# Optimization experiments

Measured on AMD Instinct MI355X. Metric: run time of the kernel, lower is better.

Reference implementation:

```python
import jax, jax.numpy as jnp
import numpy as np

B, T, D, H = 512, 128, 128, 256


def _uniform(key, shape, fan):
    s = 1.0 / np.sqrt(fan)
    return jax.random.uniform(key, shape, minval=-s, maxval=s, dtype=jnp.float32)


def setup_inputs() -> dict:
    key = jax.random.key(0)
    ks = jax.random.split(key, 16)
    return {
        "x": jax.random.normal(ks[0], (B, T, D), jnp.float32),
        "mask": jax.random.randint(ks[1], (B, T, D), 0, 2).astype(jnp.int32),
        # nn.LSTMCell(2D, H): weights init U(-1/sqrt(H), 1/sqrt(H))
        "W_ih": _uniform(ks[2], (4 * H, 2 * D), H),
        "W_hh": _uniform(ks[3], (4 * H, H), H),
        "b_ih": _uniform(ks[4], (4 * H,), H),
        "b_hh": _uniform(ks[5], (4 * H,), H),
        # TemporalDecay h: W [H, D], stdv = 1/sqrt(W.size(0)) = 1/sqrt(H)
        "W_dh": _uniform(ks[6], (H, D), H),
        "b_dh": _uniform(ks[7], (H,), H),
        # TemporalDecay x (diag): W [D, D]
        "W_dx": _uniform(ks[8], (D, D), D),
        "b_dx": _uniform(ks[9], (D,), D),
        # hist_reg Linear(H, D): torch default U(-1/sqrt(H), 1/sqrt(H))
        "W_hr": _uniform(ks[10], (D, H), H),
        "b_hr": _uniform(ks[11], (D,), H),
        "W_fr": _uniform(ks[12], (D, D), D),
        "b_fr": _uniform(ks[13], (D,), D),
        # weight_combine Linear(2D, D)
        "W_wc": _uniform(ks[14], (D, 2 * D), 2 * D),
        "b_wc": _uniform(ks[15], (D,), 2 * D),
    }


def _compute_delta(m_tm):
    # m_tm: [T, B, D] float; delta[0]=0, delta[t]=m[t-1] + (1-m[t-1])*(delta[t-1]+1)
    Tn, Bn, Dn = m_tm.shape
    def step(prev, m_prev):
        new = m_prev + (1.0 - m_prev) * (prev + 1.0)
        return new, new
    _, rest = jax.lax.scan(step, jnp.zeros((Bn, Dn), m_tm.dtype), m_tm[:-1])
    return jnp.concatenate([jnp.zeros((1, Bn, Dn), m_tm.dtype), rest], axis=0)


def _rits_forward(x, mask, W_ih, W_hh, b_ih, b_hh, W_dh, b_dh, W_dx, b_dx,
                  W_hr, b_hr, W_fr, b_fr, W_wc, b_wc):
    Bn, Tn, Dn = x.shape
    Hn = W_hh.shape[1]
    m = mask.astype(x.dtype)
    x_tm = jnp.swapaxes(x, 0, 1)   # [T,B,D]
    m_tm = jnp.swapaxes(m, 0, 1)   # [T,B,D]
    deltas = _compute_delta(m_tm)  # [T,B,D]

    W_fr_masked = W_fr * (1.0 - jnp.eye(Dn, dtype=x.dtype))  # zero diagonal
    dx_diag = jnp.diag(W_dx)  # diag-masked linear == elementwise scale

    def step(carry, inputs):
        h, c = carry
        xt, mt, dt = inputs
        gamma_h = jnp.exp(-jax.nn.relu(dt @ W_dh.T + b_dh))      # [B,H]
        gamma_x = jnp.exp(-jax.nn.relu(dt * dx_diag + b_dx))     # [B,D]
        h = h * gamma_h
        x_h = h @ W_hr.T + b_hr                                  # [B,D]
        x_c = jnp.where(mt > 0, xt, x_h)
        z_h = x_c @ W_fr_masked.T + b_fr                         # [B,D]
        alpha = jnp.concatenate([gamma_x, mt], axis=1) @ W_wc.T + b_wc
        c_h = alpha * z_h + (1.0 - alpha) * x_h
        c_c = jnp.where(mt > 0, xt, c_h)
        lstm_in = jnp.concatenate([c_c, mt], axis=1)             # [B,2D]
        gates = lstm_in @ W_ih.T + b_ih + h @ W_hh.T + b_hh      # [B,4H]
        i, f, g, o = jnp.split(gates, 4, axis=1)
        c_new = jax.nn.sigmoid(f) * c + jax.nn.sigmoid(i) * jnp.tanh(g)
        h_new = jax.nn.sigmoid(o) * jnp.tanh(c_new)
        return (h_new, c_new), (x_h, z_h, c_h)

    init = (jnp.zeros((Bn, Hn), x.dtype), jnp.zeros((Bn, Hn), x.dtype))
    _, (first, second, third) = jax.lax.scan(step, init, (x_tm, m_tm, deltas))
    first = jnp.swapaxes(first, 0, 1)
    second = jnp.swapaxes(second, 0, 1)
    third = jnp.swapaxes(third, 0, 1)
    return first, second, third, third  # x_out == third (both are c_h)


def reference(x, mask, W_ih, W_hh, b_ih, b_hh, W_dh, b_dh, W_dx, b_dx,
              W_hr, b_hr, W_fr, b_fr, W_wc, b_wc):
    return _rits_forward(x, mask, W_ih, W_hh, b_ih, b_hh, W_dh, b_dh,
                         W_dx, b_dx, W_hr, b_hr, W_fr, b_fr, W_wc, b_wc)
```

## Files before the change

### kernel.cpp

```cpp
#include <hip/hip_runtime.h>

typedef unsigned short u16;
typedef unsigned int u32;
typedef unsigned long long u64;
typedef __attribute__((ext_vector_type(8))) short s16x8;
typedef __attribute__((ext_vector_type(4))) float f32x4;

#define MFMA16(a, b, c) __builtin_amdgcn_mfma_f32_16x16x32_bf16((a), (b), (c), 0, 0, 0)

static constexpr int Bn = 512, Tn = 128, Dn = 128, Hn = 256;
static constexpr int NG = 4 * Hn;
static constexpr int KG = 2 * Dn + Hn;
static constexpr long long BTD = (long long)Bn * Tn * Dn;

__device__ __forceinline__ u16 f2bf(float f) {
  union { float f; unsigned u; } v; v.f = f;
  unsigned u = v.u;
  return (u16)((u + 0x7fffu + ((u >> 16) & 1u)) >> 16);
}
__device__ __forceinline__ float bf2f(u16 h) {
  union { unsigned u; float f; } v; v.u = ((unsigned)h) << 16;
  return v.f;
}
__device__ __forceinline__ float sigm(float x) {
  return __builtin_amdgcn_rcpf(1.f + __expf(-x));
}
__device__ __forceinline__ float ftanh(float x) {
  return 1.f - 2.f * __builtin_amdgcn_rcpf(1.f + __expf(2.f * x));
}

__global__ void k_pack(const float* __restrict__ W_ih, const float* __restrict__ W_hh,
                       const float* __restrict__ W_hr, const float* __restrict__ W_fr,
                       const float* __restrict__ W_dh, const float* __restrict__ W_wc,
                       u16* Wg, u16* Whr_b, u16* Wfr_b, u16* Wdh_b, u16* Wwc_b) {
  int i = blockIdx.x * 256 + threadIdx.x;
  if (i < NG * KG) {
    int n = i >> 9, k = i & 511;
    float v = (k < 256) ? W_ih[n * 256 + k] : W_hh[n * 256 + (k - 256)];
    Wg[i] = f2bf(v);
  }
  if (i < Dn * Hn) Whr_b[i] = f2bf(W_hr[i]);
  if (i < Dn * Dn) {
    int r = i >> 7, c = i & 127;
    Wfr_b[i] = f2bf(r == c ? 0.f : W_fr[i]);
  }
  if (i < Hn * Dn) Wdh_b[i] = f2bf(W_dh[i]);
  if (i < Dn * Hn) Wwc_b[i] = f2bf(W_wc[i]);
}

__global__ void k_delta(const float* __restrict__ x, const int* __restrict__ mask,
                        const float* __restrict__ W_dx, const float* __restrict__ b_dx,
                        u16* delta_bf, u16* gx_bf, u16* m_bf, u16* x_bf) {
  int idx = blockIdx.x * 256 + threadIdx.x;
  int b = idx >> 7, d = idx & 127;
  float dxd = W_dx[d * Dn + d], bxd = b_dx[d];
  float del = 0.f;
  const float* xrow = x + (long long)b * Tn * Dn + d;
  const int* mrow = mask + (long long)b * Tn * Dn + d;
  for (int t0 = 0; t0 < Tn; t0 += 4) {
    float xv[4]; int mv[4];
#pragma unroll
    for (int k = 0; k < 4; ++k) {
      xv[k] = xrow[(t0 + k) * Dn];
      mv[k] = mrow[(t0 + k) * Dn];
    }
#pragma unroll
    for (int k = 0; k < 4; ++k) {
      int t = t0 + k;
      long long o = ((long long)t * Bn + b) * Dn + d;
      delta_bf[o] = f2bf(del);
      gx_bf[o] = f2bf(__expf(-fmaxf(del * dxd + bxd, 0.f)));
      float m = (float)mv[k];
      m_bf[o] = f2bf(m);
      x_bf[o] = f2bf(xv[k]);
      del = m + (1.f - m) * (del + 1.f);
    }
  }
}

__global__ void k_ga(const u16* __restrict__ delta_bf, const u16* __restrict__ gx_bf,
                     const u16* __restrict__ m_bf,
                     const u16* __restrict__ Wdh_b, const u16* __restrict__ Wwc_b,
                     const float* __restrict__ b_dh, const float* __restrict__ b_wc,
                     u16* __restrict__ gammah, u16* __restrict__ alpha) {
  int tid = threadIdx.x, wid = tid >> 6, l = tid & 63;
  int lr = l & 15, lg = l >> 4;
  if (blockIdx.x < 4096) {
    int bid = blockIdx.x;
    int t = bid >> 5, b0 = (bid & 31) << 4;
    const u16* Arow = delta_bf + ((long long)t * Bn + b0) * Dn;
    s16x8 afr[4];
#pragma unroll
    for (int ks = 0; ks < 4; ++ks)
      afr[ks] = *(const s16x8*)(Arow + (long long)lr * Dn + ks * 32 + lg * 8);
#pragma unroll
    for (int q = 0; q < 4; ++q) {
      int n0 = (wid * 4 + q) * 16;
      f32x4 acc = {0.f, 0.f, 0.f, 0.f};
#pragma unroll
      for (int ks = 0; ks < 4; ++ks) {
        s16x8 bfr = *(const s16x8*)(Wdh_b + (long long)(n0 + lr) * Dn + ks * 32 + lg * 8);
        acc = MFMA16(afr[ks], bfr, acc);
      }
      int n = n0 + lr;
      float bb = b_dh[n];
#pragma unroll
      for (int r = 0; r < 4; ++r) {
        int row = lg * 4 + r;
        float g = __expf(-fmaxf(acc[r] + bb, 0.f));
        gammah[((long long)t * Bn + b0 + row) * Hn + n] = f2bf(g);
      }
    }
  } else {
    int bid = blockIdx.x - 4096;
    int t = bid >> 5, b0 = (bid & 31) << 4;
    s16x8 afr[8];
#pragma unroll
    for (int ks = 0; ks < 8; ++ks) {
      const u16* src = (ks < 4) ? gx_bf : m_bf;
      int kk = (ks & 3) * 32 + lg * 8;
      afr[ks] = *(const s16x8*)(src + ((long long)t * Bn + b0 + lr) * Dn + kk);
    }
#pragma unroll
    for (int q = 0; q < 2; ++q) {
      int n0 = (wid * 2 + q) * 16;
      f32x4 acc = {0.f, 0.f, 0.f, 0.f};
#pragma unroll
      for (int ks = 0; ks < 8; ++ks) {
        s16x8 bfr = *(const s16x8*)(Wwc_b + (long long)(n0 + lr) * (2 * Dn) + ks * 32 + lg * 8);
        acc = MFMA16(afr[ks], bfr, acc);
      }
      int n = n0 + lr;
      float bb = b_wc[n];
#pragma unroll
      for (int r = 0; r < 4; ++r)
        alpha[((long long)t * Bn + b0 + lg * 4 + r) * Dn + n] = f2bf(acc[r] + bb);
    }
  }
}

__global__ __launch_bounds__(512) void k_main(
    const u16* __restrict__ x_bf, const u16* __restrict__ m_bf,
    const u16* __restrict__ Wg, const u16* __restrict__ Whr_b, const u16* __restrict__ Wfr_b,
    const u16* __restrict__ gammah, const u16* __restrict__ alpha,
    const float* __restrict__ b_ih, const float* __restrict__ b_hh,
    const float* __restrict__ b_hr, const float* __restrict__ b_fr,
    float* __restrict__ out, u64* __restrict__ Hex, int* __restrict__ flags) {
  __shared__ __align__(16) u16 A_lds[64 * 128];
  __shared__ __align__(16) u16 Axc[16 * 128];
  __shared__ __align__(16) float G_lds[16 * 128];

  const int tid = threadIdx.x, wid = tid >> 6, l = tid & 63;
  const int lr = l & 15, lg = l >> 4;
  const int g = blockIdx.x & 31, s = blockIdx.x >> 5;
  const int b0 = g * 16;

  for (int i = tid; i < 32 * 128; i += 512) A_lds[32 * 128 + i] = 0;

  const int dd = wid * 16 + lr;
  const float bhr = b_hr[dd], bfr = b_fr[dd];

  const int prow = tid >> 5, pjj = tid & 31;
  const int pj = 32 * s + pjj;
  const float bg0 = b_ih[0 * 256 + pj] + b_hh[0 * 256 + pj];
  const float bg1 = b_ih[1 * 256 + pj] + b_hh[1 * 256 + pj];
  const float bg2 = b_ih[2 * 256 + pj] + b_hh[2 * 256 + pj];
  const float bg3 = b_ih[3 * 256 + pj] + b_hh[3 * 256 + pj];

  s16x8 whr[8], wfr[4], wg[16];
#pragma unroll
  for (int ks = 0; ks < 8; ++ks)
    whr[ks] = *(const s16x8*)(Whr_b + (long long)dd * Hn + ks * 32 + lg * 8);
#pragma unroll
  for (int ks = 0; ks < 4; ++ks)
    wfr[ks] = *(const s16x8*)(Wfr_b + (long long)dd * Dn + ks * 32 + lg * 8);
  {
    const int q = wid >> 1;
    const long long grow = q * 256 + 32 * s + 16 * (wid & 1) + lr;
#pragma unroll
    for (int ks = 0; ks < 16; ++ks)
      wg[ks] = *(const s16x8*)(Wg + grow * KG + ks * 32 + lg * 8);
  }

  const u16* a_base = A_lds + lg * 128 + lr * 8;
  const u16* axc_base = Axc + lg * 128 + lr * 8;

  float cst = 0.f;
  float xn[4], mnv[4], an[4];
#pragma unroll
  for (int r = 0; r < 4; ++r) {
    int row = lg * 4 + r;
    long long o = ((long long)0 * Bn + b0 + row) * Dn + dd;
    xn[r] = bf2f(x_bf[o]); mnv[r] = bf2f(m_bf[o]); an[r] = bf2f(alpha[o]);
  }

  float* out0 = out;
  float* out1 = out + BTD;
  float* out2 = out + 2 * BTD;
  float* out3 = out + 3 * BTD;

#pragma unroll 1
  for (int t = 0; t < Tn; ++t) {
    __syncthreads();
    float gmh = 1.f;
    if (t + 1 < Tn)
      gmh = bf2f(gammah[((long long)(t + 1) * Bn + b0 + prow) * Hn + pj]);

    f32x4 acc = {0.f, 0.f, 0.f, 0.f};
#pragma unroll
    for (int ks = 0; ks < 8; ++ks) {
      s16x8 a = *(const s16x8*)(a_base + 32 * 128 + ks * 512);
      acc = MFMA16(a, whr[ks], acc);
    }
    float xh[4], xv[4], av[4], mv[4];
#pragma unroll
    for (int r = 0; r < 4; ++r) {
      int row = lg * 4 + r;
      xh[r] = acc[r] + bhr;
      xv[r] = xn[r]; mv[r] = mnv[r]; av[r] = an[r];
      float xc = (mv[r] > 0.5f) ? xv[r] : xh[r];
      Axc[(dd >> 3) * 128 + row * 8 + (dd & 7)] = f2bf(xc);
      A_lds[(16 + (dd >> 3)) * 128 + row * 8 + (dd & 7)] = f2bf(mv[r]);
    }
    __syncthreads();

    acc = f32x4{0.f, 0.f, 0.f, 0.f};
#pragma unroll
    for (int ks = 0; ks < 4; ++ks) {
      s16x8 a = *(const s16x8*)(axc_base + ks * 512);
      acc = MFMA16(a, wfr[ks], acc);
    }
    float zv[4], chv[4];
#pragma unroll
    for (int r = 0; r < 4; ++r) {
      int row = lg * 4 + r;
      zv[r] = acc[r] + bfr;
      chv[r] = av[r] * zv[r] + (1.f - av[r]) * xh[r];
      float ccv = (mv[r] > 0.5f) ? xv[r] : chv[r];
      A_lds[(dd >> 3) * 128 + row * 8 + (dd & 7)] = f2bf(ccv);
    }
    __syncthreads();

    if (t + 1 < Tn) {
#pragma unroll
      for (int r = 0; r < 4; ++r) {
        int row = lg * 4 + r;
        long long o = ((long long)(t + 1) * Bn + b0 + row) * Dn + dd;
        xn[r] = bf2f(x_bf[o]); mnv[r] = bf2f(m_bf[o]); an[r] = bf2f(alpha[o]);
      }
    }
    acc = f32x4{0.f, 0.f, 0.f, 0.f};
#pragma unroll
    for (int ks = 0; ks < 16; ++ks) {
      s16x8 a = *(const s16x8*)(a_base + ks * 512);
      acc = MFMA16(a, wg[ks], acc);
    }
#pragma unroll
    for (int r = 0; r < 4; ++r)
      G_lds[(lg * 4 + r) * 128 + wid * 16 + lr] = acc[r];
    __syncthreads();

    float gi = G_lds[prow * 128 + 0 * 32 + pjj] + bg0;
    float gf = G_lds[prow * 128 + 1 * 32 + pjj] + bg1;
    float gg = G_lds[prow * 128 + 2 * 32 + pjj] + bg2;
    float go = G_lds[prow * 128 + 3 * 32 + pjj] + bg3;
    float iv = sigm(gi), fv = sigm(gf), gv = ftanh(gg), ov = sigm(go);
    cst = fv * cst + iv * gv;
    float h = ov * ftanh(cst);

    if (t + 1 < Tn) {
      unsigned hv = (unsigned)f2bf(h * gmh);
      unsigned up = (unsigned)__shfl_xor((int)hv, 1);
      u32* HexW = (u32*)(Hex + (size_t)((t + 1) & 1) * 32768 + (size_t)g * 1024);
      if (!(tid & 1))
        __hip_atomic_store(HexW + (prow * 128 + 16 * s + (pjj >> 1)), hv | (up << 16),
                           __ATOMIC_RELAXED, __HIP_MEMORY_SCOPE_AGENT);
      A_lds[(32 + (pj >> 3)) * 128 + prow * 8 + (pj & 7)] = (u16)hv;
      __syncthreads();
      if (tid == 0)
        __hip_atomic_store(flags + (((g << 3) | s) << 5), t + 1,
                           __ATOMIC_RELAXED, __HIP_MEMORY_SCOPE_AGENT);
    }

    if (wid == s) {
#pragma unroll
      for (int r = 0; r < 4; ++r) {
        int row = lg * 4 + r;
        long long gx = ((long long)(b0 + row) * Tn + t) * Dn + dd;
        out0[gx] = xh[r];
        out1[gx] = zv[r];
        out2[gx] = chv[r];
        out3[gx] = chv[r];
      }
    }

    if (t + 1 < Tn && wid != s) {
      const int target = t + 1;
      const int* fp = flags + (((g << 3) | wid) << 5);
      int v;
      do {
        v = __hip_atomic_load(fp, __ATOMIC_RELAXED, __HIP_MEMORY_SCOPE_AGENT);
      } while (v < target);
      const int row = l & 15, c = 4 * wid + (l >> 4);
      const u64* rp = Hex + (size_t)((t + 1) & 1) * 32768 + (size_t)g * 1024
                      + (row * 64 + c * 2);
      u64 w0 = __hip_atomic_load(rp, __ATOMIC_RELAXED, __HIP_MEMORY_SCOPE_AGENT);
      u64 w1 = __hip_atomic_load(rp + 1, __ATOMIC_RELAXED, __HIP_MEMORY_SCOPE_AGENT);
      u64* dst = (u64*)(A_lds + (32 + c) * 128 + row * 8);
      dst[0] = w0; dst[1] = w1;
    }
  }
}

extern "C" void kernel_launch(void* const* d_in, const int* in_sizes, int n_in,
                              void* d_out, int out_size, void* d_ws, size_t ws_size,
                              hipStream_t stream) {
  (void)in_sizes; (void)n_in; (void)out_size; (void)ws_size;
  const float* x = (const float*)d_in[0];
  const int* mask = (const int*)d_in[1];
  const float* W_ih = (const float*)d_in[2];
  const float* W_hh = (const float*)d_in[3];
  const float* b_ih = (const float*)d_in[4];
  const float* b_hh = (const float*)d_in[5];
  const float* W_dh = (const float*)d_in[6];
  const float* b_dh = (const float*)d_in[7];
  const float* W_dx = (const float*)d_in[8];
  const float* b_dx = (const float*)d_in[9];
  const float* W_hr = (const float*)d_in[10];
  const float* b_hr = (const float*)d_in[11];
  const float* W_fr = (const float*)d_in[12];
  const float* b_fr = (const float*)d_in[13];
  const float* W_wc = (const float*)d_in[14];
  const float* b_wc = (const float*)d_in[15];

  char* ws = (char*)d_ws;
  size_t off = 0;
  auto alloc = [&](size_t bytes) {
    void* p = ws + off;
    off = (off + bytes + 255) & ~(size_t)255;
    return p;
  };
  const long long TBD = (long long)Tn * Bn * Dn;
  const long long TBH = (long long)Tn * Bn * Hn;
  u16* delta_bf = (u16*)alloc(TBD * 2);
  u16* gx_bf    = (u16*)alloc(TBD * 2);
  u16* m_bf     = (u16*)alloc(TBD * 2);
  u16* x_bf     = (u16*)alloc(TBD * 2);
  u16* gammah   = (u16*)alloc(TBH * 2);
  u16* alphaw   = (u16*)alloc(TBD * 2);
  u16* Wg    = (u16*)alloc((size_t)NG * KG * 2);
  u16* Whr_b = (u16*)alloc((size_t)Dn * Hn * 2);
  u16* Wfr_b = (u16*)alloc((size_t)Dn * Dn * 2);
  u16* Wdh_b = (u16*)alloc((size_t)Hn * Dn * 2);
  u16* Wwc_b = (u16*)alloc((size_t)Dn * Hn * 2);

  u64* Hex = (u64*)delta_bf;
  int* flags = (int*)((char*)delta_bf + 512 * 1024);

  k_pack<<<2048, 256, 0, stream>>>(W_ih, W_hh, W_hr, W_fr, W_dh, W_wc,
                                   Wg, Whr_b, Wfr_b, Wdh_b, Wwc_b);
  k_delta<<<(Bn * Dn) / 256, 256, 0, stream>>>(x, mask, W_dx, b_dx,
                                               delta_bf, gx_bf, m_bf, x_bf);
  k_ga<<<8192, 256, 0, stream>>>(delta_bf, gx_bf, m_bf, Wdh_b, Wwc_b,
                                 b_dh, b_wc, gammah, alphaw);
  hipMemsetAsync(flags, 0, 256 * 128, stream);

  void* args[] = {
    (void*)&x_bf, (void*)&m_bf, (void*)&Wg, (void*)&Whr_b, (void*)&Wfr_b,
    (void*)&gammah, (void*)&alphaw, (void*)&b_ih, (void*)&b_hh,
    (void*)&b_hr, (void*)&b_fr, (void*)&d_out, (void*)&Hex, (void*)&flags
  };
  hipLaunchCooperativeKernel((const void*)k_main, dim3(256), dim3(512), args, 0, stream);
}
```

Measured before the change: 540.5 us.

## Fuse weight bf16 packing into consumers and reuse weight fragments across timesteps

Removes the separate k_pack launch. Each consumer kernel now reads the fp32 weights and converts them to bf16 fragments in registers, masking the W_fr diagonal inline and selecting W_ih or W_hh by column. k_ga is restructured so each block handles four timesteps with its weight fragments held in registers, which cuts the grid from 8192 to 2048 blocks and reduces redundant weight loads. The cost is more fp32 global reads and conversion work in each block's prologue, plus a serial loop over timesteps inside each k_ga block.

After: 540.7 us. Within noise of the previous version (+0.0%).

```diff
diff --git a/kernel.cpp b/kernel.cpp
--- a/kernel.cpp
+++ b/kernel.cpp
@@ -9,8 +9,6 @@
 #define MFMA16(a, b, c) __builtin_amdgcn_mfma_f32_16x16x32_bf16((a), (b), (c), 0, 0, 0)
 
 static constexpr int Bn = 512, Tn = 128, Dn = 128, Hn = 256;
-static constexpr int NG = 4 * Hn;
-static constexpr int KG = 2 * Dn + Hn;
 static constexpr long long BTD = (long long)Bn * Tn * Dn;
 
 __device__ __forceinline__ u16 f2bf(float f) {
@@ -28,24 +26,11 @@
 __device__ __forceinline__ float ftanh(float x) {
   return 1.f - 2.f * __builtin_amdgcn_rcpf(1.f + __expf(2.f * x));
 }
-
-__global__ void k_pack(const float* __restrict__ W_ih, const float* __restrict__ W_hh,
-                       const float* __restrict__ W_hr, const float* __restrict__ W_fr,
-                       const float* __restrict__ W_dh, const float* __restrict__ W_wc,
-                       u16* Wg, u16* Whr_b, u16* Wfr_b, u16* Wdh_b, u16* Wwc_b) {
-  int i = blockIdx.x * 256 + threadIdx.x;
-  if (i < NG * KG) {
-    int n = i >> 9, k = i & 511;
-    float v = (k < 256) ? W_ih[n * 256 + k] : W_hh[n * 256 + (k - 256)];
-    Wg[i] = f2bf(v);
-  }
-  if (i < Dn * Hn) Whr_b[i] = f2bf(W_hr[i]);
-  if (i < Dn * Dn) {
-    int r = i >> 7, c = i & 127;
-    Wfr_b[i] = f2bf(r == c ? 0.f : W_fr[i]);
-  }
-  if (i < Hn * Dn) Wdh_b[i] = f2bf(W_dh[i]);
-  if (i < Dn * Hn) Wwc_b[i] = f2bf(W_wc[i]);
+__device__ __forceinline__ s16x8 cvt8(const float* __restrict__ p) {
+  s16x8 v;
+#pragma unroll
+  for (int j = 0; j < 8; ++j) v[j] = (short)f2bf(p[j]);
+  return v;
 }
 
 __global__ void k_delta(const float* __restrict__ x, const int* __restrict__ mask,
@@ -80,68 +65,89 @@
 
 __global__ void k_ga(const u16* __restrict__ delta_bf, const u16* __restrict__ gx_bf,
                      const u16* __restrict__ m_bf,
-                     const u16* __restrict__ Wdh_b, const u16* __restrict__ Wwc_b,
+                     const float* __restrict__ W_dh, const float* __restrict__ W_wc,
                      const float* __restrict__ b_dh, const float* __restrict__ b_wc,
                      u16* __restrict__ gammah, u16* __restrict__ alpha) {
   int tid = threadIdx.x, wid = tid >> 6, l = tid & 63;
   int lr = l & 15, lg = l >> 4;
-  if (blockIdx.x < 4096) {
+  if (blockIdx.x < 1024) {
     int bid = blockIdx.x;
-    int t = bid >> 5, b0 = (bid & 31) << 4;
-    const u16* Arow = delta_bf + ((long long)t * Bn + b0) * Dn;
-    s16x8 afr[4];
-#pragma unroll
-    for (int ks = 0; ks < 4; ++ks)
-      afr[ks] = *(const s16x8*)(Arow + (long long)lr * Dn + ks * 32 + lg * 8);
+    int tt = (bid >> 5) * 4, b0 = (bid & 31) << 4;
+    s16x8 bfr[4][4];
 #pragma unroll
     for (int q = 0; q < 4; ++q) {
       int n0 = (wid * 4 + q) * 16;
-      f32x4 acc = {0.f, 0.f, 0.f, 0.f};
-#pragma unroll
-      for (int ks = 0; ks < 4; ++ks) {
-        s16x8 bfr = *(const s16x8*)(Wdh_b + (long long)(n0 + lr) * Dn + ks * 32 + lg * 8);
-        acc = MFMA16(afr[ks], bfr, acc);
-      }
-      int n = n0 + lr;
-      float bb = b_dh[n];
-#pragma unroll
-      for (int r = 0; r < 4; ++r) {
-        int row = lg * 4 + r;
-        float g = __expf(-fmaxf(acc[r] + bb, 0.f));
-        gammah[((long long)t * Bn + b0 + row) * Hn + n] = f2bf(g);
+#pragma unroll
+      for (int ks = 0; ks < 4; ++ks)
+        bfr[q][ks] = cvt8(W_dh + (long long)(n0 + lr) * Dn + ks * 32 + lg * 8);
+    }
+#pragma unroll 1
+    for (int k = 0; k < 4; ++k) {
+      int t = tt + k;
+      const u16* Arow = delta_bf + ((long long)t * Bn + b0) * Dn;
+      s16x8 afr[4];
+#pragma unroll
+      for (int ks = 0; ks < 4; ++ks)
+        afr[ks] = *(const s16x8*)(Arow + (long long)lr * Dn + ks * 32 + lg * 8);
+#pragma unroll
+      for (int q = 0; q < 4; ++q) {
+        int n0 = (wid * 4 + q) * 16;
+        f32x4 acc = {0.f, 0.f, 0.f, 0.f};
+#pragma unroll
+        for (int ks = 0; ks < 4; ++ks)
+          acc = MFMA16(afr[ks], bfr[q][ks], acc);
+        int n = n0 + lr;
+        float bb = b_dh[n];
+#pragma unroll
+        for (int r = 0; r < 4; ++r) {
+          int row = lg * 4 + r;
+          float g = __expf(-fmaxf(acc[r] + bb, 0.f));
+          gammah[((long long)t * Bn + b0 + row) * Hn + n] = f2bf(g);
+        }
       }
     }
   } else {
-    int bid = blockIdx.x - 4096;
-    int t = bid >> 5, b0 = (bid & 31) << 4;
-    s16x8 afr[8];
-#pragma unroll
-    for (int ks = 0; ks < 8; ++ks) {
-      const u16* src = (ks < 4) ? gx_bf : m_bf;
-      int kk = (ks & 3) * 32 + lg * 8;
-      afr[ks] = *(const s16x8*)(src + ((long long)t * Bn + b0 + lr) * Dn + kk);
-    }
+    int bid = blockIdx.x - 1024;
+    int tt = (bid >> 5) * 4, b0 = (bid & 31) << 4;
+    s16x8 bfr[2][8];
 #pragma unroll
     for (int q = 0; q < 2; ++q) {
       int n0 = (wid * 2 + q) * 16;
-      f32x4 acc = {0.f, 0.f, 0.f, 0.f};
+#pragma unroll
+      for (int ks = 0; ks < 8; ++ks)
+        bfr[q][ks] = cvt8(W_wc + (long long)(n0 + lr) * (2 * Dn) + ks * 32 + lg * 8);
+    }
+#pragma unroll 1
+    for (int k = 0; k < 4; ++k) {
+      int t = tt + k;
+      s16x8 afr[8];
 #pragma unroll
       for (int ks = 0; ks < 8; ++ks) {
-        s16x8 bfr = *(const s16x8*)(Wwc_b + (long long)(n0 + lr) * (2 * Dn) + ks * 32 + lg * 8);
-        acc = MFMA16(afr[ks], bfr, acc);
-      }
-      int n = n0 + lr;
-      float bb = b_wc[n];
-#pragma unroll
-      for (int r = 0; r < 4; ++r)
-        alpha[((long long)t * Bn + b0 + lg * 4 + r) * Dn + n] = f2bf(acc[r] + bb);
+        const u16* src = (ks < 4) ? gx_bf : m_bf;
+        afr[ks] = *(const s16x8*)(src + ((long long)t * Bn + b0 + lr) * Dn
+                                  + (ks & 3) * 32 + lg * 8);
+      }
+#pragma unroll
+      for (int q = 0; q < 2; ++q) {
+        int n0 = (wid * 2 + q) * 16;
+        f32x4 acc = {0.f, 0.f, 0.f, 0.f};
+#pragma unroll
+        for (int ks = 0; ks < 8; ++ks)
+          acc = MFMA16(afr[ks], bfr[q][ks], acc);
+        int n = n0 + lr;
+        float bb = b_wc[n];
+#pragma unroll
+        for (int r = 0; r < 4; ++r)
+          alpha[((long long)t * Bn + b0 + lg * 4 + r) * Dn + n] = f2bf(acc[r] + bb);
+      }
     }
   }
 }
 
 __global__ __launch_bounds__(512) void k_main(
     const u16* __restrict__ x_bf, const u16* __restrict__ m_bf,
-    const u16* __restrict__ Wg, const u16* __restrict__ Whr_b, const u16* __restrict__ Wfr_b,
+    const float* __restrict__ W_ih, const float* __restrict__ W_hh,
+    const float* __restrict__ W_hr, const float* __restrict__ W_fr,
     const u16* __restrict__ gammah, const u16* __restrict__ alpha,
     const float* __restrict__ b_ih, const float* __restrict__ b_hh,
     const float* __restrict__ b_hr, const float* __restrict__ b_fr,
@@ -170,16 +176,26 @@
   s16x8 whr[8], wfr[4], wg[16];
 #pragma unroll
   for (int ks = 0; ks < 8; ++ks)
-    whr[ks] = *(const s16x8*)(Whr_b + (long long)dd * Hn + ks * 32 + lg * 8);
-#pragma unroll
-  for (int ks = 0; ks < 4; ++ks)
-    wfr[ks] = *(const s16x8*)(Wfr_b + (long long)dd * Dn + ks * 32 + lg * 8);
+    whr[ks] = cvt8(W_hr + (long long)dd * Hn + ks * 32 + lg * 8);
+#pragma unroll
+  for (int ks = 0; ks < 4; ++ks) {
+    int col = ks * 32 + lg * 8;
+    s16x8 v = cvt8(W_fr + (long long)dd * Dn + col);
+#pragma unroll
+    for (int j = 0; j < 8; ++j)
+      if (col + j == dd) v[j] = 0;
+    wfr[ks] = v;
+  }
   {
     const int q = wid >> 1;
     const long long grow = q * 256 + 32 * s + 16 * (wid & 1) + lr;
 #pragma unroll
-    for (int ks = 0; ks < 16; ++ks)
-      wg[ks] = *(const s16x8*)(Wg + grow * KG + ks * 32 + lg * 8);
+    for (int ks = 0; ks < 16; ++ks) {
+      int col = ks * 32 + lg * 8;
+      const float* src = (col < 256) ? (W_ih + grow * 256 + col)
+                                     : (W_hh + grow * 256 + (col - 256));
+      wg[ks] = cvt8(src);
+    }
   }
 
   const u16* a_base = A_lds + lg * 128 + lr * 8;
@@ -348,26 +364,19 @@
   u16* x_bf     = (u16*)alloc(TBD * 2);
   u16* gammah   = (u16*)alloc(TBH * 2);
   u16* alphaw   = (u16*)alloc(TBD * 2);
-  u16* Wg    = (u16*)alloc((size_t)NG * KG * 2);
-  u16* Whr_b = (u16*)alloc((size_t)Dn * Hn * 2);
-  u16* Wfr_b = (u16*)alloc((size_t)Dn * Dn * 2);
-  u16* Wdh_b = (u16*)alloc((size_t)Hn * Dn * 2);
-  u16* Wwc_b = (u16*)alloc((size_t)Dn * Hn * 2);
 
   u64* Hex = (u64*)delta_bf;
   int* flags = (int*)((char*)delta_bf + 512 * 1024);
 
-  k_pack<<<2048, 256, 0, stream>>>(W_ih, W_hh, W_hr, W_fr, W_dh, W_wc,
-                                   Wg, Whr_b, Wfr_b, Wdh_b, Wwc_b);
   k_delta<<<(Bn * Dn) / 256, 256, 0, stream>>>(x, mask, W_dx, b_dx,
                                                delta_bf, gx_bf, m_bf, x_bf);
-  k_ga<<<8192, 256, 0, stream>>>(delta_bf, gx_bf, m_bf, Wdh_b, Wwc_b,
+  k_ga<<<2048, 256, 0, stream>>>(delta_bf, gx_bf, m_bf, W_dh, W_wc,
                                  b_dh, b_wc, gammah, alphaw);
   hipMemsetAsync(flags, 0, 256 * 128, stream);
 
   void* args[] = {
-    (void*)&x_bf, (void*)&m_bf, (void*)&Wg, (void*)&Whr_b, (void*)&Wfr_b,
-    (void*)&gammah, (void*)&alphaw, (void*)&b_ih, (void*)&b_hh,
+    (void*)&x_bf, (void*)&m_bf, (void*)&W_ih, (void*)&W_hh, (void*)&W_hr,
+    (void*)&W_fr, (void*)&gammah, (void*)&alphaw, (void*)&b_ih, (void*)&b_hh,
     (void*)&b_hr, (void*)&b_fr, (void*)&d_out, (void*)&Hex, (void*)&flags
   };
   hipLaunchCooperativeKernel((const void*)k_main, dim3(256), dim3(512), args, 0, stream);
```
